# Kernel tuning notes

Measured on AMD Instinct MI355X. Metric: run time of the kernel, lower is better.

Reference implementation:

```python
import jax, jax.numpy as jnp
import numpy as np

B, MT, D, H, DEPTH, FF = 1024, 64, 512, 8, 4, 2048
HD = D // H
N_OBJ, N_TRI = 8192, 10240
NUM_OBJ_VOCAB, NUM_PRED_VOCAB = 180, 47


def setup_inputs() -> dict:
    key = jax.random.key(0)
    ks = jax.random.split(key, 20)
    s = 0.02
    inp = {}
    inp["objs"] = jax.random.randint(ks[0], (N_OBJ,), 0, NUM_OBJ_VOCAB)
    inp["boxes"] = jax.random.uniform(ks[1], (N_OBJ, 4), dtype=jnp.float32)
    inp["triples"] = jax.random.randint(ks[2], (N_TRI, 3), 0, NUM_PRED_VOCAB)
    inp["obj_to_img"] = jnp.sort(jax.random.randint(ks[3], (N_OBJ,), 0, B))
    inp["triple_to_img"] = jnp.sort(jax.random.randint(ks[4], (N_TRI,), 0, B))
    inp["obj_emb"] = jax.random.normal(ks[5], (NUM_OBJ_VOCAB, D), jnp.float32) * s
    inp["pred_emb"] = jax.random.normal(ks[6], (NUM_PRED_VOCAB, D), jnp.float32) * s
    inp["bw1"] = jax.random.normal(ks[7], (4, D), jnp.float32) * s
    inp["bb1"] = jnp.zeros((D,), jnp.float32)
    inp["blg"] = jnp.ones((D,), jnp.float32)
    inp["blb"] = jnp.zeros((D,), jnp.float32)
    inp["bw2"] = jax.random.normal(ks[8], (D, D), jnp.float32) * s
    inp["bb2"] = jnp.zeros((D,), jnp.float32)
    inp["ln1g"] = jnp.ones((DEPTH, D), jnp.float32)
    inp["ln1b"] = jnp.zeros((DEPTH, D), jnp.float32)
    inp["wq"] = jax.random.normal(ks[9], (DEPTH, D, D), jnp.float32) * s
    inp["bq"] = jnp.zeros((DEPTH, D), jnp.float32)
    inp["wk"] = jax.random.normal(ks[10], (DEPTH, D, D), jnp.float32) * s
    inp["bk"] = jnp.zeros((DEPTH, D), jnp.float32)
    inp["wv"] = jax.random.normal(ks[11], (DEPTH, D, D), jnp.float32) * s
    inp["bv"] = jnp.zeros((DEPTH, D), jnp.float32)
    inp["wo"] = jax.random.normal(ks[12], (DEPTH, D, D), jnp.float32) * s
    inp["bo"] = jnp.zeros((DEPTH, D), jnp.float32)
    inp["ln2g"] = jnp.ones((DEPTH, D), jnp.float32)
    inp["ln2b"] = jnp.zeros((DEPTH, D), jnp.float32)
    inp["wf1"] = jax.random.normal(ks[13], (DEPTH, D, FF), jnp.float32) * s
    inp["bf1"] = jnp.zeros((DEPTH, FF), jnp.float32)
    inp["wf2"] = jax.random.normal(ks[14], (DEPTH, FF, D), jnp.float32) * s
    inp["bf2"] = jnp.zeros((DEPTH, D), jnp.float32)
    return inp


def _ln(x, g, b):
    m = x.mean(-1, keepdims=True)
    v = x.var(-1, keepdims=True)
    return (x - m) / jnp.sqrt(v + 1e-5) * g + b


def _forward(boxes, obj_emb, pred_emb, bw1, bb1, blg, blb, bw2, bb2,
             ln1g, ln1b, wq, bq, wk, bk, wv, bv, wo, bo, ln2g, ln2b,
             wf1, bf1, wf2, bf2, objs, triples, triple_to_img):
    # object tokens: embedding + box MLP (Linear -> LN -> GELU -> Linear)
    h = _ln(boxes @ bw1 + bb1, blg, blb)
    box_feat = jax.nn.gelu(h, approximate=False) @ bw2 + bb2
    obj_tok = obj_emb[objs] + box_feat  # (N_OBJ, D)

    s_idx, p_idx, o_idx = triples[:, 0], triples[:, 1], triples[:, 2]
    trip_tok = jnp.stack([obj_tok[s_idx], pred_emb[p_idx], obj_tok[o_idx]], axis=1)  # (T, 3, D)

    # vectorized ragged -> padded scatter (replaces per-image python loop)
    T = triples.shape[0]
    first = jnp.searchsorted(triple_to_img, jnp.arange(B))  # start of each image's segment
    pos = jnp.arange(T) - first[triple_to_img]               # rank of triple within its image
    slots = pos[:, None] * 3 + jnp.arange(3)[None, :]        # (T, 3) token slot per s/p/o
    imgs = jnp.broadcast_to(triple_to_img[:, None], slots.shape).reshape(-1)
    slot_c = jnp.where(slots < MT, slots, MT).reshape(-1)    # overflow -> dummy slot MT (truncation)
    tokens = jnp.zeros((B, MT + 1, D), boxes.dtype).at[imgs, slot_c].set(
        trip_tok.reshape(-1, D))[:, :MT]                     # (B, MT, D)
    mask = jnp.zeros((B, MT + 1), bool).at[imgs, slot_c].set(True)[:, :MT]  # (B, MT)

    x = tokens
    kmask = mask[:, None, None, :]  # (B,1,1,MT) valid-key mask
    scale = 1.0 / float(HD) ** 0.5
    for l in range(DEPTH):
        # pre-norm self-attention with key padding mask
        h = _ln(x, ln1g[l], ln1b[l])
        q = (h @ wq[l] + bq[l]).reshape(B, MT, H, HD)
        k = (h @ wk[l] + bk[l]).reshape(B, MT, H, HD)
        v = (h @ wv[l] + bv[l]).reshape(B, MT, H, HD)
        sc = jnp.einsum('bqhd,bkhd->bhqk', q, k) * scale
        sc = jnp.where(kmask, sc, -1e9)
        a = jax.nn.softmax(sc, axis=-1)
        attn = jnp.einsum('bhqk,bkhd->bqhd', a, v).reshape(B, MT, D)
        x = x + attn @ wo[l] + bo[l]
        # pre-norm FFN with exact GELU
        h = _ln(x, ln2g[l], ln2b[l])
        x = x + jax.nn.gelu(h @ wf1[l] + bf1[l], approximate=False) @ wf2[l] + bf2[l]
    return x


def reference(objs, boxes, triples, obj_to_img, triple_to_img, obj_emb, pred_emb,
              bw1, bb1, blg, blb, bw2, bb2, ln1g, ln1b, wq, bq, wk, bk, wv, bv,
              wo, bo, ln2g, ln2b, wf1, bf1, wf2, bf2):
    del obj_to_img  # only used in torch to derive batch_size; B is static here
    return _forward(boxes, obj_emb, pred_emb, bw1, bb1, blg, blb, bw2, bb2,
                    ln1g, ln1b, wq, bq, wk, bk, wv, bv, wo, bo, ln2g, ln2b,
                    wf1, bf1, wf2, bf2, objs, triples, triple_to_img)
```

## Files before the change

### kernel.cpp

```cpp
#include <hip/hip_runtime.h>

typedef unsigned short u16;
typedef __attribute__((ext_vector_type(8))) short s16x8;
typedef __attribute__((ext_vector_type(4))) float f32x4;

#define NB    1024
#define MTOK  64
#define DM    512
#define NHD   8
#define HDIM  64
#define FFD   2048
#define NOBJ  8192
#define NTRI  10240

__device__ __forceinline__ float bfu2f(u16 u) { return __uint_as_float(((unsigned)u) << 16); }
__device__ __forceinline__ u16 f2bfu(float f) {
  unsigned u = __float_as_uint(f);
  u += 0x7FFFu + ((u >> 16) & 1u);
  return (u16)(u >> 16);
}
__device__ __forceinline__ float gelu_exact(float x) {
  return 0.5f * x * (1.0f + erff(x * 0.70710678118654752440f));
}

__global__ void transpose_dd_kernel(const float* __restrict__ wq, const float* __restrict__ wk,
                                    const float* __restrict__ wv, const float* __restrict__ wo,
                                    u16* __restrict__ wqkvt, u16* __restrict__ wot) {
  __shared__ u16 tile[32][33];
  int l = blockIdx.z >> 2, w = blockIdx.z & 3;
  const float* src = (w == 0 ? wq : w == 1 ? wk : w == 2 ? wv : wo) + (size_t)l * 262144;
  u16* dst = (w < 3) ? (wqkvt + (size_t)l * 786432 + (size_t)w * 262144) : (wot + (size_t)l * 262144);
  int c0 = blockIdx.x * 32, r0 = blockIdx.y * 32;
  int tx = threadIdx.x, ty = threadIdx.y;
  #pragma unroll
  for (int i = 0; i < 4; i++)
    tile[ty + i * 8][tx] = f2bfu(src[(size_t)(r0 + ty + i * 8) * 512 + c0 + tx]);
  __syncthreads();
  #pragma unroll
  for (int i = 0; i < 4; i++)
    dst[(size_t)(c0 + ty + i * 8) * 512 + r0 + tx] = tile[tx][ty + i * 8];
}

__global__ void transpose_gen_kernel(const float* __restrict__ src, u16* __restrict__ dst,
                                     int R, int C) {
  __shared__ u16 tile[32][33];
  size_t mat = blockIdx.z;
  const float* s = src + mat * (size_t)R * C;
  u16* d = dst + mat * (size_t)R * C;
  int c0 = blockIdx.x * 32, r0 = blockIdx.y * 32;
  int tx = threadIdx.x, ty = threadIdx.y;
  #pragma unroll
  for (int i = 0; i < 4; i++)
    tile[ty + i * 8][tx] = f2bfu(s[(size_t)(r0 + ty + i * 8) * C + c0 + tx]);
  __syncthreads();
  #pragma unroll
  for (int i = 0; i < 4; i++)
    d[(size_t)(c0 + ty + i * 8) * R + r0 + tx] = tile[tx][ty + i * 8];
}

__global__ void concat_bias_kernel(const float* __restrict__ bq, const float* __restrict__ bk,
                                   const float* __restrict__ bv, float* __restrict__ bqkv) {
  int i = blockIdx.x * 256 + threadIdx.x;
  int l = i / 1536, j = i - l * 1536;
  int w = j >> 9, d = j & 511;
  const float* s = (w == 0) ? bq : (w == 1 ? bk : bv);
  bqkv[i] = s[l * 512 + d];
}

__global__ void first_kernel(const int* __restrict__ tti, int* __restrict__ first) {
  int b = threadIdx.x;
  int lo = 0, hi = NTRI;
  while (lo < hi) { int mid = (lo + hi) >> 1; if (tti[mid] < b) lo = mid + 1; else hi = mid; }
  first[b] = lo;
}

__global__ __launch_bounds__(256) void boxmlp_kernel(
    const int* __restrict__ objs, const float* __restrict__ boxes,
    const float* __restrict__ bw1, const float* __restrict__ bb1,
    const float* __restrict__ blg, const float* __restrict__ blb,
    const float* __restrict__ bw2, const float* __restrict__ bb2,
    const float* __restrict__ obj_emb, float* __restrict__ obj_tok) {
  __shared__ float hbuf[16][512];
  int tid = threadIdx.x;
  int base = blockIdx.x * 16;
  for (int o = 0; o < 16; o++) {
    int obj = base + o;
    float b0 = boxes[obj * 4 + 0], b1 = boxes[obj * 4 + 1];
    float b2 = boxes[obj * 4 + 2], b3 = boxes[obj * 4 + 3];
    for (int d = tid; d < 512; d += 256)
      hbuf[o][d] = bb1[d] + b0 * bw1[d] + b1 * bw1[512 + d] + b2 * bw1[1024 + d] + b3 * bw1[1536 + d];
  }
  __syncthreads();
  int wave = tid >> 6, lane = tid & 63;
  for (int oo = 0; oo < 4; oo++) {
    int o = wave * 4 + oo;
    float v[8], s = 0.f, ss = 0.f;
    #pragma unroll
    for (int e = 0; e < 8; e++) { v[e] = hbuf[o][lane * 8 + e]; s += v[e]; ss += v[e] * v[e]; }
    for (int off = 32; off > 0; off >>= 1) { s += __shfl_xor(s, off); ss += __shfl_xor(ss, off); }
    float mean = s * (1.0f / 512.0f);
    float var = ss * (1.0f / 512.0f) - mean * mean;
    float rstd = rsqrtf(var + 1e-5f);
    #pragma unroll
    for (int e = 0; e < 8; e++) {
      int d = lane * 8 + e;
      float g = (v[e] - mean) * rstd * blg[d] + blb[d];
      hbuf[o][d] = gelu_exact(g);
    }
  }
  __syncthreads();
  float acc0[16], acc1[16];
  #pragma unroll
  for (int o = 0; o < 16; o++) { acc0[o] = 0.f; acc1[o] = 0.f; }
  int d0 = tid, d1 = tid + 256;
  for (int k = 0; k < 512; k += 4) {
    float w0[4], w1[4];
    #pragma unroll
    for (int kk = 0; kk < 4; kk++) { w0[kk] = bw2[(k + kk) * 512 + d0]; w1[kk] = bw2[(k + kk) * 512 + d1]; }
    #pragma unroll
    for (int o = 0; o < 16; o++) {
      float4 hv = *(const float4*)&hbuf[o][k];
      acc0[o] += hv.x * w0[0] + hv.y * w0[1] + hv.z * w0[2] + hv.w * w0[3];
      acc1[o] += hv.x * w1[0] + hv.y * w1[1] + hv.z * w1[2] + hv.w * w1[3];
    }
  }
  #pragma unroll
  for (int o = 0; o < 16; o++) {
    int obj = base + o;
    int e = objs[obj];
    obj_tok[(size_t)obj * 512 + d0] = acc0[o] + bb2[d0] + obj_emb[(size_t)e * 512 + d0];
    obj_tok[(size_t)obj * 512 + d1] = acc1[o] + bb2[d1] + obj_emb[(size_t)e * 512 + d1];
  }
}

__global__ __launch_bounds__(128) void scatter_kernel(
    const int* __restrict__ triples, const int* __restrict__ tti,
    const int* __restrict__ first, const float* __restrict__ obj_tok,
    const float* __restrict__ pred_emb, float* __restrict__ x,
    unsigned char* __restrict__ maskb) {
  int t = blockIdx.x / 3, j = blockIdx.x - t * 3;
  int b = tti[t];
  int pos = t - first[b];
  int slot = pos * 3 + j;
  if (slot >= MTOK) return;
  int dst_row = b * MTOK + slot;
  int d = threadIdx.x * 4;
  float4 val;
  if (j == 1) {
    int p = triples[t * 3 + 1];
    val = *(const float4*)(pred_emb + (size_t)p * 512 + d);
  } else {
    int oi = triples[t * 3 + (j == 0 ? 0 : 2)];
    val = *(const float4*)(obj_tok + (size_t)oi * 512 + d);
  }
  *(float4*)(x + (size_t)dst_row * 512 + d) = val;
  if (threadIdx.x == 0) maskb[dst_row] = 1;
}

__global__ __launch_bounds__(256) void ln_kernel(
    const float* __restrict__ x, u16* __restrict__ out,
    const float* __restrict__ gg, const float* __restrict__ bb) {
  int row = blockIdx.x * 4 + (threadIdx.x >> 6);
  int lane = threadIdx.x & 63;
  const float* xr = x + (size_t)row * DM + lane * 8;
  float4 a = *(const float4*)xr;
  float4 c = *(const float4*)(xr + 4);
  float v[8] = {a.x, a.y, a.z, a.w, c.x, c.y, c.z, c.w};
  float s = 0.f, ss = 0.f;
  #pragma unroll
  for (int e = 0; e < 8; e++) { s += v[e]; ss += v[e] * v[e]; }
  for (int off = 32; off > 0; off >>= 1) { s += __shfl_xor(s, off); ss += __shfl_xor(ss, off); }
  float mean = s * (1.0f / 512.0f);
  float var = ss * (1.0f / 512.0f) - mean * mean;
  float rstd = rsqrtf(var + 1e-5f);
  int dbase = lane * 8;
  unsigned pk[4];
  #pragma unroll
  for (int p = 0; p < 4; p++) {
    float y0 = (v[2 * p] - mean) * rstd * gg[dbase + 2 * p] + bb[dbase + 2 * p];
    float y1 = (v[2 * p + 1] - mean) * rstd * gg[dbase + 2 * p + 1] + bb[dbase + 2 * p + 1];
    pk[p] = (unsigned)f2bfu(y0) | ((unsigned)f2bfu(y1) << 16);
  }
  uint4 o; o.x = pk[0]; o.y = pk[1]; o.z = pk[2]; o.w = pk[3];
  *(uint4*)(out + (size_t)row * DM + dbase) = o;
}

template <int MODE>
__global__ __launch_bounds__(256, 2) void gemm_kernel(
    const u16* __restrict__ A, const u16* __restrict__ Wt,
    const float* __restrict__ bias, float* __restrict__ resid,
    u16* __restrict__ outb, int M, int N, int K, int nb_n) {
  __shared__ u16 aT[256 * 64];
  __shared__ u16 bT[128 * 64];
  const int tid = threadIdx.x;
  const int wave = tid >> 6, lane = tid & 63;
  const int l15 = lane & 15, q4 = lane >> 4;
  const int wm = (wave >> 1) * 128, wn = (wave & 1) * 64;

  const int L = blockIdx.x;
  const int xg = L & 7, g = L >> 3;
  const int cblk = g % nb_n;
  const int pblk = xg + 8 * (g / nb_n);
  const int m0 = pblk * 256;
  const int n0 = cblk * 128;

  const int lrow = lane >> 3;
  const int scol = (((lane & 7) ^ lrow) << 3);
  const int swz = l15 & 7;

  f32x4 zero4 = {0.f, 0.f, 0.f, 0.f};
  f32x4 acc[8][4];
  #pragma unroll
  for (int i = 0; i < 8; i++)
    #pragma unroll
    for (int j = 0; j < 4; j++) acc[i][j] = zero4;

  for (int k0 = 0; k0 < K; k0 += 64) {
    __syncthreads();
    #pragma unroll
    for (int i = 0; i < 8; i++) {
      const int chunk = i * 4 + wave;
      const int row = chunk * 8 + lrow;
      __builtin_amdgcn_global_load_lds(
          (const __attribute__((address_space(1))) unsigned*)(A + (size_t)(m0 + row) * K + k0 + scol),
          (__attribute__((address_space(3))) unsigned*)(aT + chunk * 512), 16, 0, 0);
    }
    #pragma unroll
    for (int i = 0; i < 4; i++) {
      const int chunk = i * 4 + wave;
      const int row = chunk * 8 + lrow;
      __builtin_amdgcn_global_load_lds(
          (const __attribute__((address_space(1))) unsigned*)(Wt + (size_t)(n0 + row) * K + k0 + scol),
          (__attribute__((address_space(3))) unsigned*)(bT + chunk * 512), 16, 0, 0);
    }
    __syncthreads();
    #pragma unroll
    for (int kk = 0; kk < 64; kk += 32) {
      const int colA = (((kk >> 3) + q4) ^ swz) << 3;
      s16x8 fb[4];
      #pragma unroll
      for (int t = 0; t < 4; t++)
        fb[t] = *(const s16x8*)(bT + (wn + t * 16 + l15) * 64 + colA);
      #pragma unroll
      for (int i = 0; i < 8; i++) {
        s16x8 fa = *(const s16x8*)(aT + (wm + i * 16 + l15) * 64 + colA);
        #pragma unroll
        for (int j = 0; j < 4; j++)
          acc[i][j] = __builtin_amdgcn_mfma_f32_16x16x32_bf16(fa, fb[j], acc[i][j], 0, 0, 0);
      }
    }
  }

  #pragma unroll
  for (int i = 0; i < 8; i++) {
    #pragma unroll
    for (int j = 0; j < 4; j++) {
      int gn = n0 + wn + j * 16 + l15;
      float bv = bias[gn];
      #pragma unroll
      for (int r = 0; r < 4; r++) {
        int gm = m0 + wm + i * 16 + q4 * 4 + r;
        float v = acc[i][j][r] + bv;
        size_t off = (size_t)gm * N + gn;
        if (MODE == 0) outb[off] = f2bfu(v);
        else if (MODE == 1) resid[off] += v;
        else outb[off] = f2bfu(gelu_exact(v));
      }
    }
  }
}

__global__ __launch_bounds__(128) void attn_kernel(
    const u16* __restrict__ qkv, const unsigned char* __restrict__ maskb,
    u16* __restrict__ attnb) {
  __shared__ u16 vt_s[2][MTOK * 72];
  __shared__ u16 sP_s[2][MTOK * 72];
  __shared__ float maskf[MTOK];

  const int tid = threadIdx.x;
  const int wave = tid >> 6, lane = tid & 63;
  const int l15 = lane & 15, q4 = lane >> 4;
  const int b = blockIdx.x >> 2;
  const int h = ((blockIdx.x & 3) << 1) + wave;
  u16* vtw = vt_s[wave];
  u16* sw = sP_s[wave];

  if (tid < MTOK) maskf[tid] = maskb[b * MTOK + tid] ? 0.0f : -1e9f;

  {
    const u16* vrow = qkv + (size_t)(b * MTOK + lane) * 1536 + 1024 + h * HDIM;
    #pragma unroll
    for (int c8 = 0; c8 < 8; ++c8) {
      s16x8 v8 = *(const s16x8*)(vrow + c8 * 8);
      #pragma unroll
      for (int e = 0; e < 8; ++e)
        vtw[(c8 * 8 + e) * 72 + lane] = (u16)v8[e];
    }
  }
  __syncthreads();

  f32x4 zero4 = {0.f, 0.f, 0.f, 0.f};
  f32x4 acc[4][4];
  #pragma unroll
  for (int i = 0; i < 4; i++)
    #pragma unroll
    for (int j = 0; j < 4; j++) acc[i][j] = zero4;

  const u16* qbase = qkv + h * HDIM;
  const u16* kbase = qkv + 512 + h * HDIM;
  #pragma unroll
  for (int kk = 0; kk < HDIM; kk += 32) {
    s16x8 fa[4], fb[4];
    #pragma unroll
    for (int t = 0; t < 4; t++) {
      fa[t] = *(const s16x8*)(qbase + (size_t)(b * MTOK + t * 16 + l15) * 1536 + kk + q4 * 8);
      fb[t] = *(const s16x8*)(kbase + (size_t)(b * MTOK + t * 16 + l15) * 1536 + kk + q4 * 8);
    }
    #pragma unroll
    for (int i = 0; i < 4; i++)
      #pragma unroll
      for (int j = 0; j < 4; j++)
        acc[i][j] = __builtin_amdgcn_mfma_f32_16x16x32_bf16(fa[i], fb[j], acc[i][j], 0, 0, 0);
  }

  float mk[4];
  #pragma unroll
  for (int j = 0; j < 4; j++) mk[j] = maskf[j * 16 + l15];

  #pragma unroll
  for (int i = 0; i < 4; i++) {
    #pragma unroll
    for (int r = 0; r < 4; r++) {
      float mx = -3.0e38f;
      #pragma unroll
      for (int j = 0; j < 4; j++) {
        float s = acc[i][j][r] * 0.125f + mk[j];
        acc[i][j][r] = s;
        mx = fmaxf(mx, s);
      }
      mx = fmaxf(mx, __shfl_xor(mx, 1));
      mx = fmaxf(mx, __shfl_xor(mx, 2));
      mx = fmaxf(mx, __shfl_xor(mx, 4));
      mx = fmaxf(mx, __shfl_xor(mx, 8));
      float sum = 0.f;
      #pragma unroll
      for (int j = 0; j < 4; j++) {
        float e = __expf(acc[i][j][r] - mx);
        acc[i][j][r] = e;
        sum += e;
      }
      sum += __shfl_xor(sum, 1);
      sum += __shfl_xor(sum, 2);
      sum += __shfl_xor(sum, 4);
      sum += __shfl_xor(sum, 8);
      float inv = 1.0f / sum;
      int row = i * 16 + q4 * 4 + r;
      #pragma unroll
      for (int j = 0; j < 4; j++)
        sw[row * 72 + j * 16 + l15] = f2bfu(acc[i][j][r] * inv);
    }
  }
  __syncthreads();

  f32x4 oacc[4][4];
  #pragma unroll
  for (int i = 0; i < 4; i++)
    #pragma unroll
    for (int j = 0; j < 4; j++) oacc[i][j] = zero4;
  #pragma unroll
  for (int kk = 0; kk < MTOK; kk += 32) {
    s16x8 fa[4], fb[4];
    #pragma unroll
    for (int t = 0; t < 4; t++) {
      fa[t] = *(const s16x8*)(sw + (t * 16 + l15) * 72 + kk + q4 * 8);
      fb[t] = *(const s16x8*)(vtw + (t * 16 + l15) * 72 + kk + q4 * 8);
    }
    #pragma unroll
    for (int i = 0; i < 4; i++)
      #pragma unroll
      for (int j = 0; j < 4; j++)
        oacc[i][j] = __builtin_amdgcn_mfma_f32_16x16x32_bf16(fa[i], fb[j], oacc[i][j], 0, 0, 0);
  }
  #pragma unroll
  for (int i = 0; i < 4; i++)
    #pragma unroll
    for (int j = 0; j < 4; j++)
      #pragma unroll
      for (int r = 0; r < 4; r++)
        attnb[(size_t)(b * MTOK + i * 16 + q4 * 4 + r) * DM + h * HDIM + j * 16 + l15] =
            f2bfu(oacc[i][j][r]);
}

extern "C" void kernel_launch(void* const* d_in, const int* in_sizes, int n_in,
                              void* d_out, int out_size, void* d_ws, size_t ws_size,
                              hipStream_t stream) {
  (void)in_sizes; (void)n_in; (void)out_size; (void)ws_size;

  const int*   objs     = (const int*)  d_in[0];
  const float* boxes    = (const float*)d_in[1];
  const int*   triples  = (const int*)  d_in[2];
  const int*   tti      = (const int*)  d_in[4];
  const float* obj_emb  = (const float*)d_in[5];
  const float* pred_emb = (const float*)d_in[6];
  const float* bw1      = (const float*)d_in[7];
  const float* bb1      = (const float*)d_in[8];
  const float* blg      = (const float*)d_in[9];
  const float* blb      = (const float*)d_in[10];
  const float* bw2      = (const float*)d_in[11];
  const float* bb2      = (const float*)d_in[12];
  const float* ln1g     = (const float*)d_in[13];
  const float* ln1b     = (const float*)d_in[14];
  const float* wq       = (const float*)d_in[15];
  const float* bq       = (const float*)d_in[16];
  const float* wk       = (const float*)d_in[17];
  const float* bk       = (const float*)d_in[18];
  const float* wv       = (const float*)d_in[19];
  const float* bv       = (const float*)d_in[20];
  const float* wo       = (const float*)d_in[21];
  const float* bo       = (const float*)d_in[22];
  const float* ln2g     = (const float*)d_in[23];
  const float* ln2b     = (const float*)d_in[24];
  const float* wf1      = (const float*)d_in[25];
  const float* bf1      = (const float*)d_in[26];
  const float* wf2      = (const float*)d_in[27];
  const float* bf2      = (const float*)d_in[28];

  float* x = (float*)d_out;

  char* w = (char*)d_ws;
  u16* h_bf    = (u16*)w;   w += 67108864;
  u16* big     = (u16*)w;   w += 268435456;
  float* obj_tok = (float*)w; w += 16777216;
  u16* wqkvt   = (u16*)w;   w += 6291456;
  u16* wot     = (u16*)w;   w += 2097152;
  u16* wf1t    = (u16*)w;   w += 8388608;
  u16* wf2t    = (u16*)w;   w += 8388608;
  float* bqkv  = (float*)w; w += 24576;
  int* first   = (int*)w;   w += 4096;
  unsigned char* maskb = (unsigned char*)w; w += 65536;

  u16* qkv_bf  = big;
  u16* attn_bf = big + 100663296UL;
  u16* ff1_bf  = big;

  hipMemsetAsync(x, 0, 134217728UL, stream);
  hipMemsetAsync(maskb, 0, 65536, stream);

  transpose_dd_kernel<<<dim3(16, 16, 16), dim3(32, 8), 0, stream>>>(wq, wk, wv, wo, wqkvt, wot);
  transpose_gen_kernel<<<dim3(64, 16, 4), dim3(32, 8), 0, stream>>>(wf1, wf1t, 512, 2048);
  transpose_gen_kernel<<<dim3(16, 64, 4), dim3(32, 8), 0, stream>>>(wf2, wf2t, 2048, 512);
  concat_bias_kernel<<<24, 256, 0, stream>>>(bq, bk, bv, bqkv);
  first_kernel<<<1, 1024, 0, stream>>>(tti, first);
  boxmlp_kernel<<<512, 256, 0, stream>>>(objs, boxes, bw1, bb1, blg, blb, bw2, bb2, obj_emb, obj_tok);
  scatter_kernel<<<NTRI * 3, 128, 0, stream>>>(triples, tti, first, obj_tok, pred_emb, x, maskb);

  for (int l = 0; l < 4; l++) {
    ln_kernel<<<16384, 256, 0, stream>>>(x, h_bf, ln1g + l * 512, ln1b + l * 512);
    gemm_kernel<0><<<256 * 12, 256, 0, stream>>>(h_bf, wqkvt + (size_t)l * 786432,
                                                 bqkv + l * 1536, nullptr, qkv_bf,
                                                 65536, 1536, 512, 12);
    attn_kernel<<<4096, 128, 0, stream>>>(qkv_bf, maskb, attn_bf);
    gemm_kernel<1><<<256 * 4, 256, 0, stream>>>(attn_bf, wot + (size_t)l * 262144,
                                                bo + l * 512, x, nullptr,
                                                65536, 512, 512, 4);
    ln_kernel<<<16384, 256, 0, stream>>>(x, h_bf, ln2g + l * 512, ln2b + l * 512);
    gemm_kernel<2><<<256 * 16, 256, 0, stream>>>(h_bf, wf1t + (size_t)l * 1048576,
                                                 bf1 + l * 2048, nullptr, ff1_bf,
                                                 65536, 2048, 512, 16);
    gemm_kernel<1><<<256 * 4, 256, 0, stream>>>(ff1_bf, wf2t + (size_t)l * 1048576,
                                                bf2 + l * 512, x, nullptr,
                                                65536, 512, 2048, 4);
  }
}
```

Measured before the change: 3.998 ms.

## Double-buffer GEMM shared-memory tiles and shrink block tile to 128x128

The bf16 MFMA GEMM now uses two shared-memory buffers for A and B. While the current K-slice is being multiplied, the next 64-wide K-slice is issued with direct global-to-LDS loads. The block tile shrinks from 256x128 to 128x128, so each wave holds 4x4 instead of 8x4 accumulators, and the launch grids double to match. The goal is to hide global load latency behind MFMA work and cut per-wave register use. The cost is lower operand reuse per block and more blocks re-reading the weight tiles.

Result: slower. 4.522 ms (+13.1%).

```diff
diff --git a/kernel.cpp b/kernel.cpp
--- a/kernel.cpp
+++ b/kernel.cpp
@@ -190,18 +190,18 @@
     const u16* __restrict__ A, const u16* __restrict__ Wt,
     const float* __restrict__ bias, float* __restrict__ resid,
     u16* __restrict__ outb, int M, int N, int K, int nb_n) {
-  __shared__ u16 aT[256 * 64];
-  __shared__ u16 bT[128 * 64];
+  __shared__ u16 aT[2][128 * 64];
+  __shared__ u16 bT[2][128 * 64];
   const int tid = threadIdx.x;
   const int wave = tid >> 6, lane = tid & 63;
   const int l15 = lane & 15, q4 = lane >> 4;
-  const int wm = (wave >> 1) * 128, wn = (wave & 1) * 64;
+  const int wm = (wave >> 1) * 64, wn = (wave & 1) * 64;
 
   const int L = blockIdx.x;
   const int xg = L & 7, g = L >> 3;
   const int cblk = g % nb_n;
   const int pblk = xg + 8 * (g / nb_n);
-  const int m0 = pblk * 256;
+  const int m0 = pblk * 128;
   const int n0 = cblk * 128;
 
   const int lrow = lane >> 3;
@@ -209,50 +209,54 @@
   const int swz = l15 & 7;
 
   f32x4 zero4 = {0.f, 0.f, 0.f, 0.f};
-  f32x4 acc[8][4];
-  #pragma unroll
-  for (int i = 0; i < 8; i++)
+  f32x4 acc[4][4];
+  #pragma unroll
+  for (int i = 0; i < 4; i++)
     #pragma unroll
     for (int j = 0; j < 4; j++) acc[i][j] = zero4;
 
-  for (int k0 = 0; k0 < K; k0 += 64) {
-    __syncthreads();
-    #pragma unroll
-    for (int i = 0; i < 8; i++) {
+  auto stage = [&](int buf, int k0) {
+    #pragma unroll
+    for (int i = 0; i < 4; i++) {
       const int chunk = i * 4 + wave;
       const int row = chunk * 8 + lrow;
       __builtin_amdgcn_global_load_lds(
           (const __attribute__((address_space(1))) unsigned*)(A + (size_t)(m0 + row) * K + k0 + scol),
-          (__attribute__((address_space(3))) unsigned*)(aT + chunk * 512), 16, 0, 0);
-    }
-    #pragma unroll
-    for (int i = 0; i < 4; i++) {
-      const int chunk = i * 4 + wave;
-      const int row = chunk * 8 + lrow;
+          (__attribute__((address_space(3))) unsigned*)(&aT[buf][chunk * 512]), 16, 0, 0);
       __builtin_amdgcn_global_load_lds(
           (const __attribute__((address_space(1))) unsigned*)(Wt + (size_t)(n0 + row) * K + k0 + scol),
-          (__attribute__((address_space(3))) unsigned*)(bT + chunk * 512), 16, 0, 0);
-    }
-    __syncthreads();
+          (__attribute__((address_space(3))) unsigned*)(&bT[buf][chunk * 512]), 16, 0, 0);
+    }
+  };
+
+  stage(0, 0);
+  __syncthreads();
+
+  const int nk = K >> 6;
+  for (int t = 0; t < nk; ++t) {
+    const int cur = t & 1;
+    if (t + 1 < nk) stage(cur ^ 1, (t + 1) << 6);
     #pragma unroll
     for (int kk = 0; kk < 64; kk += 32) {
       const int colA = (((kk >> 3) + q4) ^ swz) << 3;
-      s16x8 fb[4];
-      #pragma unroll
-      for (int t = 0; t < 4; t++)
-        fb[t] = *(const s16x8*)(bT + (wn + t * 16 + l15) * 64 + colA);
-      #pragma unroll
-      for (int i = 0; i < 8; i++) {
-        s16x8 fa = *(const s16x8*)(aT + (wm + i * 16 + l15) * 64 + colA);
+      s16x8 fb[4], fa[4];
+      #pragma unroll
+      for (int j = 0; j < 4; j++)
+        fb[j] = *(const s16x8*)(&bT[cur][(wn + j * 16 + l15) * 64 + colA]);
+      #pragma unroll
+      for (int i = 0; i < 4; i++)
+        fa[i] = *(const s16x8*)(&aT[cur][(wm + i * 16 + l15) * 64 + colA]);
+      #pragma unroll
+      for (int i = 0; i < 4; i++)
         #pragma unroll
         for (int j = 0; j < 4; j++)
-          acc[i][j] = __builtin_amdgcn_mfma_f32_16x16x32_bf16(fa, fb[j], acc[i][j], 0, 0, 0);
-      }
-    }
-  }
-
-  #pragma unroll
-  for (int i = 0; i < 8; i++) {
+          acc[i][j] = __builtin_amdgcn_mfma_f32_16x16x32_bf16(fa[i], fb[j], acc[i][j], 0, 0, 0);
+    }
+    __syncthreads();
+  }
+
+  #pragma unroll
+  for (int i = 0; i < 4; i++) {
     #pragma unroll
     for (int j = 0; j < 4; j++) {
       int gn = n0 + wn + j * 16 + l15;
@@ -456,18 +460,18 @@
 
   for (int l = 0; l < 4; l++) {
     ln_kernel<<<16384, 256, 0, stream>>>(x, h_bf, ln1g + l * 512, ln1b + l * 512);
-    gemm_kernel<0><<<256 * 12, 256, 0, stream>>>(h_bf, wqkvt + (size_t)l * 786432,
+    gemm_kernel<0><<<512 * 12, 256, 0, stream>>>(h_bf, wqkvt + (size_t)l * 786432,
                                                  bqkv + l * 1536, nullptr, qkv_bf,
                                                  65536, 1536, 512, 12);
     attn_kernel<<<4096, 128, 0, stream>>>(qkv_bf, maskb, attn_bf);
-    gemm_kernel<1><<<256 * 4, 256, 0, stream>>>(attn_bf, wot + (size_t)l * 262144,
+    gemm_kernel<1><<<512 * 4, 256, 0, stream>>>(attn_bf, wot + (size_t)l * 262144,
                                                 bo + l * 512, x, nullptr,
                                                 65536, 512, 512, 4);
     ln_kernel<<<16384, 256, 0, stream>>>(x, h_bf, ln2g + l * 512, ln2b + l * 512);
-    gemm_kernel<2><<<256 * 16, 256, 0, stream>>>(h_bf, wf1t + (size_t)l * 1048576,
+    gemm_kernel<2><<<512 * 16, 256, 0, stream>>>(h_bf, wf1t + (size_t)l * 1048576,
                                                  bf1 + l * 2048, nullptr, ff1_bf,
                                                  65536, 2048, 512, 16);
-    gemm_kernel<1><<<256 * 4, 256, 0, stream>>>(ff1_bf, wf2t + (size_t)l * 1048576,
+    gemm_kernel<1><<<512 * 4, 256, 0, stream>>>(ff1_bf, wf2t + (size_t)l * 1048576,
                                                 bf2 + l * 512, x, nullptr,
                                                 65536, 512, 2048, 4);
   }
```
